# Kernel optimization log

Measured on AMD Instinct MI355X. Metric: run time of the kernel, lower is better.

The kernel has to match this reference:

```python
import jax, jax.numpy as jnp
import numpy as np

B = 512       # batch/feature rows
N = 131072    # node dimension (last axis of x)
E = 131072    # edges per tree level
L = 4         # number of tree levels


def setup_inputs() -> dict:
    key = jax.random.key(0)
    kx, k0, k1, k2, k3 = jax.random.split(key, 5)
    x = jax.random.normal(kx, (B, N), dtype=jnp.float32)
    edges0 = jax.random.randint(k0, (2, E), 0, N, dtype=jnp.int64)
    edges1 = jax.random.randint(k1, (2, E), 0, N, dtype=jnp.int64)
    edges2 = jax.random.randint(k2, (2, E), 0, N, dtype=jnp.int64)
    edges3 = jax.random.randint(k3, (2, E), 0, N, dtype=jnp.int64)
    return {"x": x, "edges0": edges0, "edges1": edges1,
            "edges2": edges2, "edges3": edges3}


def reference(x, edges0, edges1, edges2, edges3):
    # TreeAggregation.forward: iterate levels from deepest (last) to root
    # (first). Per level: gather x at src along last dim, scatter-add into
    # dst (duplicate dst indices accumulate, matching torch.index_add).
    for edges in (edges3, edges2, edges1, edges0):
        src = edges[0, :]
        dst = edges[1, :]
        values = x[:, src]                 # [B, E] gather
        x = x.at[:, dst].add(values)       # scatter-add with duplicates
    return x
```

## Files before the change

kernel.cpp:

```cpp
#include <hip/hip_runtime.h>
#include <hip/hip_bf16.h>

#define BATCH 512
#define NNODE 131072
#define NEDGE 131072
#define NLAYER 4
#define SCAN_BLK 1024
#define SCAN_NBLK (NNODE / SCAN_BLK)
#define PCAP (8 * NEDGE)

__device__ int g_counts[NLAYER][NNODE];
__device__ int g_offs[NLAYER][NNODE];
__device__ int g_cursor[NLAYER][NNODE];
__device__ int g_srcl[NLAYER][NEDGE];
__device__ int g_bsums[NLAYER][SCAN_NBLK];

__device__ int p_cnt[2][NNODE];
__device__ int p_offs[2][NNODE];
__device__ int p_srcl[2][PCAP];
__device__ int p_bsums[2][SCAN_NBLK];

__device__ int s_hist[2][64], s_cur[2][64];
__device__ int d_perm[2][NNODE];

typedef unsigned int uivec4 __attribute__((ext_vector_type(4)));
typedef float fvec4 __attribute__((ext_vector_type(4)));

__device__ __forceinline__ void nt_store_u4(uint4* p, uint4 v) {
    uivec4 w = {v.x, v.y, v.z, v.w};
    __builtin_nontemporal_store(w, reinterpret_cast<uivec4*>(p));
}

__device__ __forceinline__ void nt_store_f4(float* p, float4 v) {
    fvec4 w = {v.x, v.y, v.z, v.w};
    __builtin_nontemporal_store(w, reinterpret_cast<fvec4*>(p));
}

__global__ void zero_counts_k() {
    int i = blockIdx.x * blockDim.x + threadIdx.x;
    ((int*)g_counts)[i] = 0;
}

__global__ void hist_k(const int* __restrict__ p0, const int* __restrict__ p1,
                       const int* __restrict__ p2, const int* __restrict__ p3) {
    int i = blockIdx.x * blockDim.x + threadIdx.x;
    int layer = i >> 17;
    int e = i & (NEDGE - 1);
    const int* eg = layer == 0 ? p0 : layer == 1 ? p1 : layer == 2 ? p2 : p3;
    atomicAdd(&g_counts[layer][eg[NEDGE + e]], 1);
}

__global__ void scan_block_k() {
    __shared__ int sh[SCAN_BLK];
    int layer = blockIdx.x / SCAN_NBLK;
    int blk = blockIdx.x % SCAN_NBLK;
    int t = threadIdx.x;
    int i = blk * SCAN_BLK + t;
    int own = g_counts[layer][i];
    sh[t] = own;
    __syncthreads();
    for (int off = 1; off < SCAN_BLK; off <<= 1) {
        int v = (t >= off) ? sh[t - off] : 0;
        __syncthreads();
        sh[t] += v;
        __syncthreads();
    }
    g_offs[layer][i] = sh[t] - own;
    if (t == SCAN_BLK - 1) g_bsums[layer][blk] = sh[t];
}

__global__ void scan_bsums_k() {
    __shared__ int sh[SCAN_NBLK];
    int layer = blockIdx.x;
    int t = threadIdx.x;
    int own = g_bsums[layer][t];
    sh[t] = own;
    __syncthreads();
    for (int off = 1; off < SCAN_NBLK; off <<= 1) {
        int v = (t >= off) ? sh[t - off] : 0;
        __syncthreads();
        sh[t] += v;
        __syncthreads();
    }
    g_bsums[layer][t] = sh[t] - own;
}

__global__ void scan_add_k() {
    int layer = blockIdx.x / SCAN_NBLK;
    int blk = blockIdx.x % SCAN_NBLK;
    int i = blk * SCAN_BLK + threadIdx.x;
    int o = g_offs[layer][i] + g_bsums[layer][blk];
    g_offs[layer][i] = o;
    g_cursor[layer][i] = o;
}

__global__ void fill_k(const int* __restrict__ p0, const int* __restrict__ p1,
                       const int* __restrict__ p2, const int* __restrict__ p3) {
    int i = blockIdx.x * blockDim.x + threadIdx.x;
    int layer = i >> 17;
    int e = i & (NEDGE - 1);
    const int* eg = layer == 0 ? p0 : layer == 1 ? p1 : layer == 2 ? p2 : p3;
    int s = eg[e];
    int d = eg[NEDGE + e];
    int p = atomicAdd(&g_cursor[layer][d], 1);
    g_srcl[layer][p] = s;
}

__global__ void count_pair_k() {
    int i = blockIdx.x * blockDim.x + threadIdx.x;
    int pr = i >> 17;
    int d = i & (NNODE - 1);
    int U = pr * 2, V = pr * 2 + 1;
    int c = 1 + g_counts[U][d];
    int vb = g_offs[V][d], vd = g_counts[V][d];
    for (int j = 0; j < vd; ++j) {
        int s = g_srcl[V][vb + j];
        c += 1 + g_counts[U][s];
    }
    p_cnt[pr][d] = c;
}

__global__ void pscan_block_k() {
    __shared__ int sh[SCAN_BLK];
    int pr = blockIdx.x / SCAN_NBLK;
    int blk = blockIdx.x % SCAN_NBLK;
    int t = threadIdx.x;
    int i = blk * SCAN_BLK + t;
    int own = p_cnt[pr][i];
    sh[t] = own;
    __syncthreads();
    for (int off = 1; off < SCAN_BLK; off <<= 1) {
        int v = (t >= off) ? sh[t - off] : 0;
        __syncthreads();
        sh[t] += v;
        __syncthreads();
    }
    p_offs[pr][i] = sh[t] - own;
    if (t == SCAN_BLK - 1) p_bsums[pr][blk] = sh[t];
}

__global__ void pscan_bsums_k() {
    __shared__ int sh[SCAN_NBLK];
    int pr = blockIdx.x;
    int t = threadIdx.x;
    int own = p_bsums[pr][t];
    sh[t] = own;
    __syncthreads();
    for (int off = 1; off < SCAN_NBLK; off <<= 1) {
        int v = (t >= off) ? sh[t - off] : 0;
        __syncthreads();
        sh[t] += v;
        __syncthreads();
    }
    p_bsums[pr][t] = sh[t] - own;
}

__global__ void pscan_add_k() {
    int pr = blockIdx.x / SCAN_NBLK;
    int blk = blockIdx.x % SCAN_NBLK;
    int i = blk * SCAN_BLK + threadIdx.x;
    p_offs[pr][i] += p_bsums[pr][blk];
}

__global__ void fill_pair_k() {
    int i = blockIdx.x * blockDim.x + threadIdx.x;
    int pr = i >> 17;
    int d = i & (NNODE - 1);
    int U = pr * 2, V = pr * 2 + 1;
    int p = p_offs[pr][d];
    int* buf = p_srcl[pr];
    buf[p++] = d;
    int ub = g_offs[U][d], ud = g_counts[U][d];
    for (int j = 0; j < ud; ++j) buf[p++] = g_srcl[U][ub + j];
    int vb = g_offs[V][d], vd = g_counts[V][d];
    for (int j = 0; j < vd; ++j) {
        int s = g_srcl[V][vb + j];
        buf[p++] = s;
        int sb = g_offs[U][s], sd = g_counts[U][s];
        for (int k = 0; k < sd; ++k) buf[p++] = g_srcl[U][sb + k];
    }
}

__global__ void sort_zero_k() {
    int t = threadIdx.x;
    ((int*)s_hist)[t] = 0;
}

__global__ void histp_k() {
    __shared__ int lh[64];
    int t = threadIdx.x;
    int pr = blockIdx.x >> 7;
    int n = (blockIdx.x & 127) * 1024 + t;
    if (t < 64) lh[t] = 0;
    __syncthreads();
    int b = 63 - min(p_cnt[pr][n], 63);
    atomicAdd(&lh[b], 1);
    __syncthreads();
    if (t < 64) atomicAdd(&s_hist[pr][t], lh[t]);
}

__global__ void sort_scan_k() {
    __shared__ int sh[2][64];
    int t = threadIdx.x;
    int pr = t >> 6;
    int k = t & 63;
    sh[pr][k] = s_hist[pr][k];
    __syncthreads();
    for (int off = 1; off < 64; off <<= 1) {
        int v = (k >= off) ? sh[pr][k - off] : 0;
        __syncthreads();
        sh[pr][k] += v;
        __syncthreads();
    }
    s_cur[pr][k] = sh[pr][k] - s_hist[pr][k];
}

__global__ void permp_k() {
    __shared__ int lh[64];
    __shared__ int lbase[64];
    int t = threadIdx.x;
    int pr = blockIdx.x >> 7;
    int n = (blockIdx.x & 127) * 1024 + t;
    if (t < 64) lh[t] = 0;
    __syncthreads();
    int b = 63 - min(p_cnt[pr][n], 63);
    int lpos = atomicAdd(&lh[b], 1);
    __syncthreads();
    if (t < 64) lbase[t] = lh[t] ? atomicAdd(&s_cur[pr][t], lh[t]) : 0;
    __syncthreads();
    d_perm[pr][lbase[b] + lpos] = n;
}

__global__ void transpose_bf_k(const float* __restrict__ in, unsigned short* __restrict__ out) {
    __shared__ float tile[64][65];
    int c0 = blockIdx.x * 64;
    int r0 = blockIdx.y * 64;
    int tx = threadIdx.x;
    int ty = threadIdx.y;
    float4 v[4];
#pragma unroll
    for (int i = 0; i < 4; ++i)
        v[i] = *reinterpret_cast<const float4*>(&in[(size_t)(r0 + ty + 16 * i) * NNODE + c0 + 4 * tx]);
#pragma unroll
    for (int i = 0; i < 4; ++i) {
        tile[ty + 16 * i][4 * tx + 0] = v[i].x;
        tile[ty + 16 * i][4 * tx + 1] = v[i].y;
        tile[ty + 16 * i][4 * tx + 2] = v[i].z;
        tile[ty + 16 * i][4 * tx + 3] = v[i].w;
    }
    __syncthreads();
#pragma unroll
    for (int i = 0; i < 4; ++i) {
        int n = c0 + ty + 16 * i;
        ushort4 w;
        __hip_bfloat16 h0 = __float2bfloat16(tile[4 * tx + 0][ty + 16 * i]);
        __hip_bfloat16 h1 = __float2bfloat16(tile[4 * tx + 1][ty + 16 * i]);
        __hip_bfloat16 h2 = __float2bfloat16(tile[4 * tx + 2][ty + 16 * i]);
        __hip_bfloat16 h3 = __float2bfloat16(tile[4 * tx + 3][ty + 16 * i]);
        w.x = *reinterpret_cast<unsigned short*>(&h0);
        w.y = *reinterpret_cast<unsigned short*>(&h1);
        w.z = *reinterpret_cast<unsigned short*>(&h2);
        w.w = *reinterpret_cast<unsigned short*>(&h3);
        *reinterpret_cast<ushort4*>(&out[(size_t)n * BATCH + r0 + 4 * tx]) = w;
    }
}

__global__ void transpose_fb_k(const unsigned short* __restrict__ in, float* __restrict__ out) {
    __shared__ float tile[64][65];
    int n0 = blockIdx.x * 64;
    int b0 = blockIdx.y * 64;
    int tx = threadIdx.x;
    int ty = threadIdx.y;
#pragma unroll
    for (int i = 0; i < 4; ++i) {
        int nl = ty + 16 * i;
        ushort4 w = *reinterpret_cast<const ushort4*>(&in[(size_t)(n0 + nl) * BATCH + b0 + 4 * tx]);
        tile[nl][4 * tx + 0] = __uint_as_float((unsigned)w.x << 16);
        tile[nl][4 * tx + 1] = __uint_as_float((unsigned)w.y << 16);
        tile[nl][4 * tx + 2] = __uint_as_float((unsigned)w.z << 16);
        tile[nl][4 * tx + 3] = __uint_as_float((unsigned)w.w << 16);
    }
    __syncthreads();
#pragma unroll
    for (int i = 0; i < 4; ++i) {
        int bl = ty + 16 * i;
        float4 w;
        w.x = tile[4 * tx + 0][bl];
        w.y = tile[4 * tx + 1][bl];
        w.z = tile[4 * tx + 2][bl];
        w.w = tile[4 * tx + 3][bl];
        nt_store_f4(&out[(size_t)(b0 + bl) * NNODE + n0 + 4 * tx], w);
    }
}

__device__ __forceinline__ void gacc8(float* a, uint4 v) {
    a[0] += __uint_as_float(v.x << 16);
    a[1] += __uint_as_float(v.x & 0xffff0000u);
    a[2] += __uint_as_float(v.y << 16);
    a[3] += __uint_as_float(v.y & 0xffff0000u);
    a[4] += __uint_as_float(v.z << 16);
    a[5] += __uint_as_float(v.z & 0xffff0000u);
    a[6] += __uint_as_float(v.w << 16);
    a[7] += __uint_as_float(v.w & 0xffff0000u);
}

__device__ __forceinline__ unsigned pack2(float lo, float hi) {
    __hip_bfloat16 l = __float2bfloat16(lo);
    __hip_bfloat16 h = __float2bfloat16(hi);
    return (unsigned)*reinterpret_cast<unsigned short*>(&l) |
           ((unsigned)*reinterpret_cast<unsigned short*>(&h) << 16);
}

__global__ void __launch_bounds__(512) gather4_k(const uint4* __restrict__ cur,
                                                 uint4* __restrict__ out, int pr) {
    int t = threadIdx.x;
    int q = t & 63;
    int wv = t >> 6;
    int base = blockIdx.x * 32 + wv * 4;
    int n[4], deg[4];
    const int* sl[4];
#pragma unroll
    for (int k = 0; k < 4; ++k) {
        n[k] = d_perm[pr][base + k];
        deg[k] = __builtin_amdgcn_readfirstlane(p_cnt[pr][n[k]]);
        sl[k] = &p_srcl[pr][p_offs[pr][n[k]]];
    }
    float acc[4][8];
#pragma unroll
    for (int k = 0; k < 4; ++k)
#pragma unroll
        for (int m = 0; m < 8; ++m) acc[k][m] = 0.f;
    int jmax = max(max(deg[0], deg[1]), max(deg[2], deg[3]));
    int j = 0;
    for (; j + 2 <= jmax; j += 2) {
        uint4 v[8];
#pragma unroll
        for (int k = 0; k < 4; ++k) {
            if (j < deg[k])     v[2 * k]     = cur[(size_t)sl[k][j] * 64 + q];
            if (j + 1 < deg[k]) v[2 * k + 1] = cur[(size_t)sl[k][j + 1] * 64 + q];
        }
#pragma unroll
        for (int k = 0; k < 4; ++k) {
            if (j < deg[k])     gacc8(acc[k], v[2 * k]);
            if (j + 1 < deg[k]) gacc8(acc[k], v[2 * k + 1]);
        }
    }
    if (j < jmax) {
        uint4 v[4];
#pragma unroll
        for (int k = 0; k < 4; ++k)
            if (j < deg[k]) v[k] = cur[(size_t)sl[k][j] * 64 + q];
#pragma unroll
        for (int k = 0; k < 4; ++k)
            if (j < deg[k]) gacc8(acc[k], v[k]);
    }
#pragma unroll
    for (int k = 0; k < 4; ++k) {
        uint4 w;
        w.x = pack2(acc[k][0], acc[k][1]);
        w.y = pack2(acc[k][2], acc[k][3]);
        w.z = pack2(acc[k][4], acc[k][5]);
        w.w = pack2(acc[k][6], acc[k][7]);
        nt_store_u4(&out[(size_t)n[k] * 64 + q], w);
    }
}

extern "C" void kernel_launch(void* const* d_in, const int* in_sizes, int n_in,
                              void* d_out, int out_size, void* d_ws, size_t ws_size,
                              hipStream_t stream) {
    const float* x = (const float*)d_in[0];
    const int* p0 = (const int*)d_in[4];
    const int* p1 = (const int*)d_in[3];
    const int* p2 = (const int*)d_in[2];
    const int* p3 = (const int*)d_in[1];

    unsigned short* WS0 = (unsigned short*)d_ws;
    unsigned short* WS1 = WS0 + (size_t)NNODE * BATCH;
    float* OUT = (float*)d_out;

    zero_counts_k<<<NLAYER * NNODE / 1024, 1024, 0, stream>>>();
    hist_k<<<NLAYER * NEDGE / 1024, 1024, 0, stream>>>(p0, p1, p2, p3);
    scan_block_k<<<NLAYER * SCAN_NBLK, SCAN_BLK, 0, stream>>>();
    scan_bsums_k<<<NLAYER, SCAN_NBLK, 0, stream>>>();
    scan_add_k<<<NLAYER * SCAN_NBLK, SCAN_BLK, 0, stream>>>();
    fill_k<<<NLAYER * NEDGE / 1024, 1024, 0, stream>>>(p0, p1, p2, p3);

    count_pair_k<<<2 * NNODE / 1024, 1024, 0, stream>>>();
    pscan_block_k<<<2 * SCAN_NBLK, SCAN_BLK, 0, stream>>>();
    pscan_bsums_k<<<2, SCAN_NBLK, 0, stream>>>();
    pscan_add_k<<<2 * SCAN_NBLK, SCAN_BLK, 0, stream>>>();
    fill_pair_k<<<2 * NNODE / 256, 256, 0, stream>>>();

    sort_zero_k<<<1, 128, 0, stream>>>();
    histp_k<<<2 * NNODE / 1024, 1024, 0, stream>>>();
    sort_scan_k<<<1, 128, 0, stream>>>();
    permp_k<<<2 * NNODE / 1024, 1024, 0, stream>>>();

    transpose_bf_k<<<dim3(NNODE / 64, BATCH / 64), dim3(16, 16), 0, stream>>>(x, WS0);

    gather4_k<<<NNODE / 32, 512, 0, stream>>>((const uint4*)WS0, (uint4*)WS1, 0);
    gather4_k<<<NNODE / 32, 512, 0, stream>>>((const uint4*)WS1, (uint4*)WS0, 1);
    transpose_fb_k<<<dim3(NNODE / 64, BATCH / 64), dim3(16, 16), 0, stream>>>(WS0, OUT);
}
```

Before: 488.6 us.

## Build paired-level CSR edge-parallel and drop degree-sorted node permutation

Only the U levels (edges0, edges2) now get a per-destination CSR. The paired counts and fills are computed edge-parallel over the V levels with atomics, replacing the per-node loops that serialised on high in-degree. The degree-bucket sort and permutation of destination nodes are removed, so the gather kernel handles nodes in natural order. This cuts preprocessing launches and load imbalance, but wavefronts may now mix nodes of very different degree, and the order of sources within each list becomes nondeterministic.

```diff
diff --git a/kernel.cpp b/kernel.cpp
--- a/kernel.cpp
+++ b/kernel.cpp
@@ -4,24 +4,21 @@
 #define BATCH 512
 #define NNODE 131072
 #define NEDGE 131072
-#define NLAYER 4
 #define SCAN_BLK 1024
 #define SCAN_NBLK (NNODE / SCAN_BLK)
 #define PCAP (8 * NEDGE)
 
-__device__ int g_counts[NLAYER][NNODE];
-__device__ int g_offs[NLAYER][NNODE];
-__device__ int g_cursor[NLAYER][NNODE];
-__device__ int g_srcl[NLAYER][NEDGE];
-__device__ int g_bsums[NLAYER][SCAN_NBLK];
+__device__ int g_counts[2][NNODE];
+__device__ int g_offs[2][NNODE];
+__device__ int g_cursor[2][NNODE];
+__device__ int g_srcl[2][NEDGE];
+__device__ int g_bsums[2][SCAN_NBLK];
 
 __device__ int p_cnt[2][NNODE];
 __device__ int p_offs[2][NNODE];
+__device__ int p_cursor[2][NNODE];
 __device__ int p_srcl[2][PCAP];
 __device__ int p_bsums[2][SCAN_NBLK];
-
-__device__ int s_hist[2][64], s_cur[2][64];
-__device__ int d_perm[2][NNODE];
 
 typedef unsigned int uivec4 __attribute__((ext_vector_type(4)));
 typedef float fvec4 __attribute__((ext_vector_type(4)));
@@ -36,27 +33,27 @@
     __builtin_nontemporal_store(w, reinterpret_cast<fvec4*>(p));
 }
 
-__global__ void zero_counts_k() {
+__global__ void zero2_k() {
     int i = blockIdx.x * blockDim.x + threadIdx.x;
     ((int*)g_counts)[i] = 0;
 }
 
-__global__ void hist_k(const int* __restrict__ p0, const int* __restrict__ p1,
-                       const int* __restrict__ p2, const int* __restrict__ p3) {
-    int i = blockIdx.x * blockDim.x + threadIdx.x;
-    int layer = i >> 17;
+__global__ void histU_k(const int* __restrict__ u0, const int* __restrict__ u1) {
+    int i = blockIdx.x * blockDim.x + threadIdx.x;
+    int pr = i >> 17;
     int e = i & (NEDGE - 1);
-    const int* eg = layer == 0 ? p0 : layer == 1 ? p1 : layer == 2 ? p2 : p3;
-    atomicAdd(&g_counts[layer][eg[NEDGE + e]], 1);
+    const int* eg = pr ? u1 : u0;
+    atomicAdd(&g_counts[pr][eg[NEDGE + e]], 1);
 }
 
 __global__ void scan_block_k() {
     __shared__ int sh[SCAN_BLK];
-    int layer = blockIdx.x / SCAN_NBLK;
+    int pr = blockIdx.x / SCAN_NBLK;
     int blk = blockIdx.x % SCAN_NBLK;
     int t = threadIdx.x;
     int i = blk * SCAN_BLK + t;
-    int own = g_counts[layer][i];
+    int own = g_counts[pr][i];
+    p_cnt[pr][i] = 1 + own;
     sh[t] = own;
     __syncthreads();
     for (int off = 1; off < SCAN_BLK; off <<= 1) {
@@ -65,15 +62,15 @@
         sh[t] += v;
         __syncthreads();
     }
-    g_offs[layer][i] = sh[t] - own;
-    if (t == SCAN_BLK - 1) g_bsums[layer][blk] = sh[t];
+    g_offs[pr][i] = sh[t] - own;
+    if (t == SCAN_BLK - 1) g_bsums[pr][blk] = sh[t];
 }
 
 __global__ void scan_bsums_k() {
     __shared__ int sh[SCAN_NBLK];
-    int layer = blockIdx.x;
-    int t = threadIdx.x;
-    int own = g_bsums[layer][t];
+    int pr = blockIdx.x;
+    int t = threadIdx.x;
+    int own = g_bsums[pr][t];
     sh[t] = own;
     __syncthreads();
     for (int off = 1; off < SCAN_NBLK; off <<= 1) {
@@ -82,42 +79,37 @@
         sh[t] += v;
         __syncthreads();
     }
-    g_bsums[layer][t] = sh[t] - own;
+    g_bsums[pr][t] = sh[t] - own;
 }
 
 __global__ void scan_add_k() {
-    int layer = blockIdx.x / SCAN_NBLK;
+    int pr = blockIdx.x / SCAN_NBLK;
     int blk = blockIdx.x % SCAN_NBLK;
     int i = blk * SCAN_BLK + threadIdx.x;
-    int o = g_offs[layer][i] + g_bsums[layer][blk];
-    g_offs[layer][i] = o;
-    g_cursor[layer][i] = o;
-}
-
-__global__ void fill_k(const int* __restrict__ p0, const int* __restrict__ p1,
-                       const int* __restrict__ p2, const int* __restrict__ p3) {
-    int i = blockIdx.x * blockDim.x + threadIdx.x;
-    int layer = i >> 17;
+    int o = g_offs[pr][i] + g_bsums[pr][blk];
+    g_offs[pr][i] = o;
+    g_cursor[pr][i] = o;
+}
+
+__global__ void fillU_k(const int* __restrict__ u0, const int* __restrict__ u1) {
+    int i = blockIdx.x * blockDim.x + threadIdx.x;
+    int pr = i >> 17;
     int e = i & (NEDGE - 1);
-    const int* eg = layer == 0 ? p0 : layer == 1 ? p1 : layer == 2 ? p2 : p3;
+    const int* eg = pr ? u1 : u0;
     int s = eg[e];
     int d = eg[NEDGE + e];
-    int p = atomicAdd(&g_cursor[layer][d], 1);
-    g_srcl[layer][p] = s;
-}
-
-__global__ void count_pair_k() {
-    int i = blockIdx.x * blockDim.x + threadIdx.x;
-    int pr = i >> 17;
-    int d = i & (NNODE - 1);
-    int U = pr * 2, V = pr * 2 + 1;
-    int c = 1 + g_counts[U][d];
-    int vb = g_offs[V][d], vd = g_counts[V][d];
-    for (int j = 0; j < vd; ++j) {
-        int s = g_srcl[V][vb + j];
-        c += 1 + g_counts[U][s];
-    }
-    p_cnt[pr][d] = c;
+    int p = atomicAdd(&g_cursor[pr][d], 1);
+    g_srcl[pr][p] = s;
+}
+
+__global__ void pedge_cnt_k(const int* __restrict__ v0, const int* __restrict__ v1) {
+    int i = blockIdx.x * blockDim.x + threadIdx.x;
+    int pr = i >> 17;
+    int e = i & (NEDGE - 1);
+    const int* eg = pr ? v1 : v0;
+    int s = eg[e];
+    int d = eg[NEDGE + e];
+    atomicAdd(&p_cnt[pr][d], 1 + g_counts[pr][s]);
 }
 
 __global__ void pscan_block_k() {
@@ -159,76 +151,35 @@
     int pr = blockIdx.x / SCAN_NBLK;
     int blk = blockIdx.x % SCAN_NBLK;
     int i = blk * SCAN_BLK + threadIdx.x;
-    p_offs[pr][i] += p_bsums[pr][blk];
-}
-
-__global__ void fill_pair_k() {
+    int o = p_offs[pr][i] + p_bsums[pr][blk];
+    p_offs[pr][i] = o;
+    p_cursor[pr][i] = o + 1 + g_counts[pr][i];
+}
+
+__global__ void pfill_base_k() {
     int i = blockIdx.x * blockDim.x + threadIdx.x;
     int pr = i >> 17;
     int d = i & (NNODE - 1);
-    int U = pr * 2, V = pr * 2 + 1;
     int p = p_offs[pr][d];
     int* buf = p_srcl[pr];
     buf[p++] = d;
-    int ub = g_offs[U][d], ud = g_counts[U][d];
-    for (int j = 0; j < ud; ++j) buf[p++] = g_srcl[U][ub + j];
-    int vb = g_offs[V][d], vd = g_counts[V][d];
-    for (int j = 0; j < vd; ++j) {
-        int s = g_srcl[V][vb + j];
-        buf[p++] = s;
-        int sb = g_offs[U][s], sd = g_counts[U][s];
-        for (int k = 0; k < sd; ++k) buf[p++] = g_srcl[U][sb + k];
-    }
-}
-
-__global__ void sort_zero_k() {
-    int t = threadIdx.x;
-    ((int*)s_hist)[t] = 0;
-}
-
-__global__ void histp_k() {
-    __shared__ int lh[64];
-    int t = threadIdx.x;
-    int pr = blockIdx.x >> 7;
-    int n = (blockIdx.x & 127) * 1024 + t;
-    if (t < 64) lh[t] = 0;
-    __syncthreads();
-    int b = 63 - min(p_cnt[pr][n], 63);
-    atomicAdd(&lh[b], 1);
-    __syncthreads();
-    if (t < 64) atomicAdd(&s_hist[pr][t], lh[t]);
-}
-
-__global__ void sort_scan_k() {
-    __shared__ int sh[2][64];
-    int t = threadIdx.x;
-    int pr = t >> 6;
-    int k = t & 63;
-    sh[pr][k] = s_hist[pr][k];
-    __syncthreads();
-    for (int off = 1; off < 64; off <<= 1) {
-        int v = (k >= off) ? sh[pr][k - off] : 0;
-        __syncthreads();
-        sh[pr][k] += v;
-        __syncthreads();
-    }
-    s_cur[pr][k] = sh[pr][k] - s_hist[pr][k];
-}
-
-__global__ void permp_k() {
-    __shared__ int lh[64];
-    __shared__ int lbase[64];
-    int t = threadIdx.x;
-    int pr = blockIdx.x >> 7;
-    int n = (blockIdx.x & 127) * 1024 + t;
-    if (t < 64) lh[t] = 0;
-    __syncthreads();
-    int b = 63 - min(p_cnt[pr][n], 63);
-    int lpos = atomicAdd(&lh[b], 1);
-    __syncthreads();
-    if (t < 64) lbase[t] = lh[t] ? atomicAdd(&s_cur[pr][t], lh[t]) : 0;
-    __syncthreads();
-    d_perm[pr][lbase[b] + lpos] = n;
+    int ub = g_offs[pr][d], ud = g_counts[pr][d];
+    for (int j = 0; j < ud; ++j) buf[p++] = g_srcl[pr][ub + j];
+}
+
+__global__ void pfill_edge_k(const int* __restrict__ v0, const int* __restrict__ v1) {
+    int i = blockIdx.x * blockDim.x + threadIdx.x;
+    int pr = i >> 17;
+    int e = i & (NEDGE - 1);
+    const int* eg = pr ? v1 : v0;
+    int s = eg[e];
+    int d = eg[NEDGE + e];
+    int cs = g_counts[pr][s];
+    int p = atomicAdd(&p_cursor[pr][d], 1 + cs);
+    int* buf = p_srcl[pr];
+    buf[p++] = s;
+    int sb = g_offs[pr][s];
+    for (int k = 0; k < cs; ++k) buf[p++] = g_srcl[pr][sb + k];
 }
 
 __global__ void transpose_bf_k(const float* __restrict__ in, unsigned short* __restrict__ out) {
@@ -317,13 +268,12 @@
     int q = t & 63;
     int wv = t >> 6;
     int base = blockIdx.x * 32 + wv * 4;
-    int n[4], deg[4];
+    int deg[4];
     const int* sl[4];
 #pragma unroll
     for (int k = 0; k < 4; ++k) {
-        n[k] = d_perm[pr][base + k];
-        deg[k] = __builtin_amdgcn_readfirstlane(p_cnt[pr][n[k]]);
-        sl[k] = &p_srcl[pr][p_offs[pr][n[k]]];
+        deg[k] = __builtin_amdgcn_readfirstlane(p_cnt[pr][base + k]);
+        sl[k] = &p_srcl[pr][p_offs[pr][base + k]];
     }
     float acc[4][8];
 #pragma unroll
@@ -361,7 +311,7 @@
         w.y = pack2(acc[k][2], acc[k][3]);
         w.z = pack2(acc[k][4], acc[k][5]);
         w.w = pack2(acc[k][6], acc[k][7]);
-        nt_store_u4(&out[(size_t)n[k] * 64 + q], w);
+        nt_store_u4(&out[(size_t)(base + k) * 64 + q], w);
     }
 }
 
@@ -369,32 +319,28 @@
                               void* d_out, int out_size, void* d_ws, size_t ws_size,
                               hipStream_t stream) {
     const float* x = (const float*)d_in[0];
-    const int* p0 = (const int*)d_in[4];
-    const int* p1 = (const int*)d_in[3];
-    const int* p2 = (const int*)d_in[2];
-    const int* p3 = (const int*)d_in[1];
+    const int* U0 = (const int*)d_in[4];
+    const int* V0 = (const int*)d_in[3];
+    const int* U1 = (const int*)d_in[2];
+    const int* V1 = (const int*)d_in[1];
 
     unsigned short* WS0 = (unsigned short*)d_ws;
     unsigned short* WS1 = WS0 + (size_t)NNODE * BATCH;
     float* OUT = (float*)d_out;
 
-    zero_counts_k<<<NLAYER * NNODE / 1024, 1024, 0, stream>>>();
-    hist_k<<<NLAYER * NEDGE / 1024, 1024, 0, stream>>>(p0, p1, p2, p3);
-    scan_block_k<<<NLAYER * SCAN_NBLK, SCAN_BLK, 0, stream>>>();
-    scan_bsums_k<<<NLAYER, SCAN_NBLK, 0, stream>>>();
-    scan_add_k<<<NLAYER * SCAN_NBLK, SCAN_BLK, 0, stream>>>();
-    fill_k<<<NLAYER * NEDGE / 1024, 1024, 0, stream>>>(p0, p1, p2, p3);
-
-    count_pair_k<<<2 * NNODE / 1024, 1024, 0, stream>>>();
+    zero2_k<<<2 * NNODE / 1024, 1024, 0, stream>>>();
+    histU_k<<<2 * NEDGE / 1024, 1024, 0, stream>>>(U0, U1);
+    scan_block_k<<<2 * SCAN_NBLK, SCAN_BLK, 0, stream>>>();
+    scan_bsums_k<<<2, SCAN_NBLK, 0, stream>>>();
+    scan_add_k<<<2 * SCAN_NBLK, SCAN_BLK, 0, stream>>>();
+    fillU_k<<<2 * NEDGE / 1024, 1024, 0, stream>>>(U0, U1);
+
+    pedge_cnt_k<<<2 * NEDGE / 1024, 1024, 0, stream>>>(V0, V1);
     pscan_block_k<<<2 * SCAN_NBLK, SCAN_BLK, 0, stream>>>();
     pscan_bsums_k<<<2, SCAN_NBLK, 0, stream>>>();
     pscan_add_k<<<2 * SCAN_NBLK, SCAN_BLK, 0, stream>>>();
-    fill_pair_k<<<2 * NNODE / 256, 256, 0, stream>>>();
-
-    sort_zero_k<<<1, 128, 0, stream>>>();
-    histp_k<<<2 * NNODE / 1024, 1024, 0, stream>>>();
-    sort_scan_k<<<1, 128, 0, stream>>>();
-    permp_k<<<2 * NNODE / 1024, 1024, 0, stream>>>();
+    pfill_base_k<<<2 * NNODE / 1024, 1024, 0, stream>>>();
+    pfill_edge_k<<<2 * NEDGE / 1024, 1024, 0, stream>>>(V0, V1);
 
     transpose_bf_k<<<dim3(NNODE / 64, BATCH / 64), dim3(16, 16), 0, stream>>>(x, WS0);
 
```

After: 497.7 us. No clear change (+1.9%).
